# Kernel tuning notes

Measured on AMD Instinct MI355X. Metric: run time of the kernel, lower is better.

## Reference

```python
import jax, jax.numpy as jnp
import numpy as np

# ---- hardware / module constants (match init_kwargs) ----
IN_BITS = 8
OUT_PREC_BITS = 8
OUT_RANGE_BITS = 4
VMAX = 0.6                      # hardware_input_vmax
I_SCALE = 8020.0                # hardware_output_current_scaling
DAC_SCALE = 1.0 / 2 ** (IN_BITS - 1)
DAC_MAX = 2 ** (IN_BITS - 1)
DAC_MIN = -DAC_MAX
ADC_SCALE = 1.0 / 2 ** OUT_PREC_BITS
ADC_MAX = 2 ** (OUT_PREC_BITS + OUT_RANGE_BITS - 1)
ADC_MIN = -ADC_MAX
BW = 1e-08
KBT = 1.380649e-23 * 300.0
E_CONST = float(np.exp(1))
V_EPS = 1e-12                   # noise_minimum_voltage
WP = 3                          # weight_precision -> L = WP-1 bit levels
L = WP - 1
MI, MO = 128, 128               # memristor tile size
TJ, TK = 2, 2                   # input/output tiling (256/128)
OUT_FEATURES = 256


def fake_quant(x, scale, qmin, qmax):
    # torch.fake_quantize_per_tensor_affine with zero_point=0 (STE grads)
    q = jnp.round(x / scale)
    y = jnp.clip(q, qmin, qmax) * scale
    mask = (q >= qmin) & (q <= qmax)
    xg = jnp.where(mask, x, jax.lax.stop_gradient(x))
    return xg + jax.lax.stop_gradient(y - xg)


def poly_eval(c, x):
    # c: [2, P] ascending-degree coeffs (pos/neg stacked), x: [B,T,I] -> [2,B,T,I]
    # Horner form: same math as sum_p c_p * x**p, grad-safe at x == 0.
    acc = jnp.broadcast_to(c[:, -1][:, None, None, None], (2,) + x.shape)
    for p in range(c.shape[-1] - 2, -1, -1):
        acc = acc * x[None] + c[:, p][:, None, None, None]
    return acc


def _paired_array(cl, ch, r, v, noise):
    # cl:[2,Pl] ch:[2,Ph] r:[2,MI,MO] v:[B,T,MI] noise:[2,T,MI,MO]
    low = poly_eval(cl, v)[..., None]       # [2,B,T,MI,1]
    high = poly_eval(ch, v)[..., None]
    r_b = r[:, None, None]                  # [2,1,1,MI,MO]
    raw = low * (1.0 - r_b) + high * r_b    # [2,B,T,MI,MO]
    johnson = 4.0 * KBT * BW * jnp.abs(raw / (jnp.abs(v)[None, ..., None] + V_EPS))
    shot = 2.0 * E_CONST * jnp.abs(raw) * BW
    sigma = jnp.sqrt(johnson + shot)
    noised = raw + noise[:, None] * sigma   # noise broadcast over batch dim B
    out = jnp.sum(noised, axis=-2)          # reduce over I -> [2,B,T,MO]
    return out[0] - out[1]                  # paired (pos - neg) bitlines


def _forward(x, poly_low, poly_high, r, bias):
    v = fake_quant(x, DAC_SCALE, DAC_MIN, DAC_MAX) * VMAX   # DAC
    B, T, _ = x.shape
    out = jnp.zeros((B, T, TK * MO), x.dtype)
    for i, bit in enumerate(reversed(range(WP - 1))):
        for j in range(TJ):
            vj = v[..., j * MI:(j + 1) * MI]
            for k in range(TK):
                nkey = jax.random.fold_in(jax.random.key(42), i * TJ * TK + j * TK + k)
                noise = jax.random.normal(nkey, (2, T, MI, MO), x.dtype)
                pair = _paired_array(poly_low[i, j, k], poly_high[i, j, k], r[i, j, k], vj, noise)
                adc_out = fake_quant(pair * I_SCALE, ADC_SCALE, ADC_MIN, ADC_MAX)  # ADC
                out = out.at[..., k * MO:(k + 1) * MO].add(adc_out * (2.0 ** bit))
    return out[..., :OUT_FEATURES] + bias


def setup_inputs() -> dict:
    key = jax.random.key(0)
    ks = jax.random.split(key, 5)
    x = jax.random.normal(ks[0], (4, 256, 256), jnp.float32)
    poly_low = jax.random.normal(ks[1], (L, TJ, TK, 2, 7), jnp.float32) * 1e-3
    poly_high = jax.random.normal(ks[2], (L, TJ, TK, 2, 6), jnp.float32) * 1e-3
    r = jax.random.uniform(ks[3], (L, TJ, TK, 2, MI, MO), dtype=jnp.float32)
    bias = jax.random.normal(ks[4], (OUT_FEATURES,), jnp.float32) * 0.01
    return {"x": x, "poly_low": poly_low, "poly_high": poly_high, "r": r, "bias": bias}


def reference(x, poly_low, poly_high, r, bias):
    return _forward(x, poly_low, poly_high, r, bias)
```

## Files before the change

kernel.cpp:

```cpp
#include <hip/hip_runtime.h>
#include <stdint.h>


struct KeyPack { uint32_t k0[8]; uint32_t k1[8]; uint32_t k2[8]; };

#define TFR(r)  { x0 += x1; \
  x1 = __builtin_amdgcn_alignbit(x1, x1, 32u - (r)); x1 ^= x0; }
#define TFR3(r, kinj) { x0 = x0 + x1 + (kinj); \
  x1 = __builtin_amdgcn_alignbit(x1, x1, 32u - (r)); x1 ^= x0; }

__device__ __forceinline__ uint32_t tf_bits(uint32_t ks0, uint32_t ks1,
                                            uint32_t ks2, uint32_t x1) {
  uint32_t x0 = ks0;
  TFR(13) TFR(15) TFR(26) TFR(6)
  x1 += ks2 + 1u;
  TFR3(17, ks1) TFR(29) TFR(16) TFR(24)
  x1 += ks0 + 2u;
  TFR3(13, ks2) TFR(15) TFR(26) TFR(6)
  x1 += ks1 + 3u;
  TFR3(17, ks0) TFR(29) TFR(16) TFR(24)
  x1 += ks2 + 4u;
  TFR3(13, ks1) TFR(15) TFR(26) TFR(6)
  x0 += ks2; x1 += ks0 + 5u;
  return x0 ^ x1;
}

__host__ inline void threefry2x32_host(uint32_t k0, uint32_t k1,
                                       uint32_t x0, uint32_t x1,
                                       uint32_t& y0, uint32_t& y1) {
  const uint32_t ks0 = k0, ks1 = k1, ks2 = k0 ^ k1 ^ 0x1BD11BDAu;
  x0 += ks0; x1 += ks1;
#define TF_ROUND(r) { x0 += x1; x1 = (x1 << (r)) | (x1 >> (32 - (r))); x1 ^= x0; }
  TF_ROUND(13) TF_ROUND(15) TF_ROUND(26) TF_ROUND(6)
  x0 += ks1; x1 += ks2 + 1u;
  TF_ROUND(17) TF_ROUND(29) TF_ROUND(16) TF_ROUND(24)
  x0 += ks2; x1 += ks0 + 2u;
  TF_ROUND(13) TF_ROUND(15) TF_ROUND(26) TF_ROUND(6)
  x0 += ks0; x1 += ks1 + 3u;
  TF_ROUND(17) TF_ROUND(29) TF_ROUND(16) TF_ROUND(24)
  x0 += ks1; x1 += ks2 + 4u;
  TF_ROUND(13) TF_ROUND(15) TF_ROUND(26) TF_ROUND(6)
  x0 += ks2; x1 += ks0 + 5u;
#undef TF_ROUND
  y0 = x0; y1 = x1;
}

__device__ __forceinline__ float bits_to_nscaled(uint32_t bits) {
  float g = __uint_as_float(__builtin_amdgcn_alignbit(0x7Fu, bits, 9u));
  float u = fmaxf(fmaf(g, 2.0f, -3.0f), -0.99999994f);
  float l = __logf(fmaf(u, -u, 1.0f));
  float p;
  if (l > -5.0f) {
    float z = -2.5f - l;
    p =            -4.134083e-7f;
    p = fmaf(p, z, -1.377554e-6f);
    p = fmaf(p, z,  8.132747e-5f);
    p = fmaf(p, z,  4.950817e-4f);
  } else {
    float z = __builtin_amdgcn_sqrtf(-l) - 3.0f;
    p =            -2.513466e-6f;
    p = fmaf(p, z,  3.112373e-6f);
    p = fmaf(p, z,  3.302966e-4f);
    p = fmaf(p, z,  9.341406e-4f);
  }
  return p * u;
}

__global__ void memristor_init(const float* __restrict__ bias,
                               float* __restrict__ out) {
  int idx = blockIdx.x * 256 + threadIdx.x;
  out[idx] = bias[idx & 255];
}

__global__ __launch_bounds__(256, 4)
void memristor_main(const float* __restrict__ x,
                    const float* __restrict__ poly_low,
                    const float* __restrict__ poly_high,
                    const float* __restrict__ r,
                    float* __restrict__ out,
                    KeyPack keys) {
  __shared__ __align__(16) float LH[128][16];
  __shared__ float RED[128][9];

  const int tid = threadIdx.x;
  const int bid = blockIdx.x;
  const int c = bid >> 8;
  const int t = bid & 255;
  const int j = (c >> 1) & 1;
  const int k = c & 1;

  for (int task = tid; task < 1024; task += 256) {
    int pb = task & 7;
    int mi = task >> 3;
    int p = pb >> 2, b = pb & 3;
    float xv = x[(b * 256 + t) * 256 + j * 128 + mi];
    float q = rintf(xv * 128.0f);
    q = fminf(fmaxf(q, -128.0f), 128.0f);
    float v = (q * 0.0078125f) * 0.6f;
    const float* cl = poly_low + (c * 2 + p) * 7;
    float lo = cl[6];
    #pragma unroll
    for (int n = 5; n >= 0; --n) lo = fmaf(lo, v, cl[n]);
    const float* ch = poly_high + (c * 2 + p) * 6;
    float hi = ch[5];
    #pragma unroll
    for (int n = 4; n >= 0; --n) hi = fmaf(hi, v, ch[n]);
    LH[mi][pb] = lo;
    LH[mi][8 + pb] = hi - lo;
  }
  __syncthreads();

  const int mo = tid & 127;
  const int mih = tid >> 7;
  const int miBase = mih * 64;
  const uint32_t k0 = keys.k0[c], k1 = keys.k1[c], k2 = keys.k2[c];
  const float* r0p = r + c * 32768 + miBase * 128 + mo;
  const float* r1p = r0p + 16384;
  uint32_t sk = (uint32_t)(t * 16384 + miBase * 128 + mo) + k1;

  float acc[8];
  #pragma unroll
  for (int v2 = 0; v2 < 8; ++v2) acc[v2] = 0.0f;

  #pragma unroll 2
  for (int ii = 0; ii < 64; ++ii) {
    const float4* lh4 = (const float4*)(&LH[miBase + ii][0]);
    float4 L0 = lh4[0];
    float4 L1 = lh4[1];
    float4 D0 = lh4[2];
    float4 D1 = lh4[3];
    float r0 = r0p[ii * 128];
    float r1 = r1p[ii * 128];

    uint32_t b0 = tf_bits(k0, k1, k2, sk);
    uint32_t b1 = tf_bits(k0, k1, k2, sk + 4194304u);
    sk += 128u;
    float n0 = bits_to_nscaled(b0);
    float n1 = bits_to_nscaled(b1);

    float raw0 = fmaf(D0.x, r0, L0.x);
    float raw1 = fmaf(D0.y, r0, L0.y);
    float raw2 = fmaf(D0.z, r0, L0.z);
    float raw3 = fmaf(D0.w, r0, L0.w);
    float raw4 = fmaf(D1.x, r1, L1.x);
    float raw5 = fmaf(D1.y, r1, L1.y);
    float raw6 = fmaf(D1.z, r1, L1.z);
    float raw7 = fmaf(D1.w, r1, L1.w);

    float q0 = __builtin_amdgcn_sqrtf(fabsf(raw0));
    float q1 = __builtin_amdgcn_sqrtf(fabsf(raw1));
    float q2 = __builtin_amdgcn_sqrtf(fabsf(raw2));
    float q3 = __builtin_amdgcn_sqrtf(fabsf(raw3));
    float q4 = __builtin_amdgcn_sqrtf(fabsf(raw4));
    float q5 = __builtin_amdgcn_sqrtf(fabsf(raw5));
    float q6 = __builtin_amdgcn_sqrtf(fabsf(raw6));
    float q7 = __builtin_amdgcn_sqrtf(fabsf(raw7));

    acc[0] += fmaf(n0, q0, raw0);
    acc[1] += fmaf(n0, q1, raw1);
    acc[2] += fmaf(n0, q2, raw2);
    acc[3] += fmaf(n0, q3, raw3);
    acc[4] += fmaf(n1, q4, raw4);
    acc[5] += fmaf(n1, q5, raw5);
    acc[6] += fmaf(n1, q6, raw6);
    acc[7] += fmaf(n1, q7, raw7);
  }

  if (mih == 1) {
    #pragma unroll
    for (int v2 = 0; v2 < 8; ++v2) RED[mo][v2] = acc[v2];
  }
  __syncthreads();
  if (mih == 0) {
    #pragma unroll
    for (int v2 = 0; v2 < 8; ++v2) acc[v2] += RED[mo][v2];
    const float QSC = 2053120.0f;
    const float OSC = (c & 4) ? 0.00390625f : 0.0078125f;
    #pragma unroll
    for (int b = 0; b < 4; ++b) {
      float pair = acc[b] - acc[4 + b];
      float q = rintf(pair * QSC);
      q = fminf(fmaxf(q, -2048.0f), 2048.0f);
      atomicAdd(&out[(b * 256 + t) * 256 + k * 128 + mo], q * OSC);
    }
  }
}

extern "C" void kernel_launch(void* const* d_in, const int* in_sizes, int n_in,
                              void* d_out, int out_size, void* d_ws, size_t ws_size,
                              hipStream_t stream) {
  const float* x    = (const float*)d_in[0];
  const float* pl   = (const float*)d_in[1];
  const float* ph   = (const float*)d_in[2];
  const float* r    = (const float*)d_in[3];
  const float* bias = (const float*)d_in[4];
  float* out = (float*)d_out;

  KeyPack keys;
  for (uint32_t cc = 0; cc < 8; ++cc) {
    uint32_t y0, y1;
    threefry2x32_host(0u, 42u, 0u, cc, y0, y1);
    keys.k0[cc] = y0; keys.k1[cc] = y1;
    keys.k2[cc] = y0 ^ y1 ^ 0x1BD11BDAu;
  }

  memristor_init<<<1024, 256, 0, stream>>>(bias, out);
  memristor_main<<<2048, 256, 0, stream>>>(x, pl, ph, r, out, keys);
}
```

Before: 220.3 us.

## Pack four time steps per 1024-thread block and use log2-based inverse-erf

Each block now handles four consecutive time steps with 1024 threads instead of one with 256, so the grid shrinks from 2048 to 512 blocks and shared LH/RED buffers are replicated per sub-block. The same r tile is read by the four sub-blocks, which may improve cache reuse and lower launch overhead. Separately, the Gaussian noise transform now uses log2 directly with refit polynomial coefficients, dropping the offset subtraction in the central branch. Launch bounds of 1024 threads with min 4 blocks per unit may force tighter register limits, and the refit coefficients risk small numerical deviations.

```diff
diff --git a/kernel.cpp b/kernel.cpp
--- a/kernel.cpp
+++ b/kernel.cpp
@@ -48,20 +48,19 @@
 __device__ __forceinline__ float bits_to_nscaled(uint32_t bits) {
   float g = __uint_as_float(__builtin_amdgcn_alignbit(0x7Fu, bits, 9u));
   float u = fmaxf(fmaf(g, 2.0f, -3.0f), -0.99999994f);
-  float l = __logf(fmaf(u, -u, 1.0f));
+  float lam = __log2f(fmaf(u, -u, 1.0f));
   float p;
-  if (l > -5.0f) {
-    float z = -2.5f - l;
-    p =            -4.134083e-7f;
-    p = fmaf(p, z, -1.377554e-6f);
-    p = fmaf(p, z,  8.132747e-5f);
-    p = fmaf(p, z,  4.950817e-4f);
+  if (lam > -7.2134752f) {
+    p =              1.376760e-7f;
+    p = fmaf(p, lam, 8.278247e-7f);
+    p = fmaf(p, lam, -5.5773259e-5f);
+    p = fmaf(p, lam, 2.8961282e-4f);
   } else {
-    float z = __builtin_amdgcn_sqrtf(-l) - 3.0f;
-    p =            -2.513466e-6f;
-    p = fmaf(p, z,  3.112373e-6f);
-    p = fmaf(p, z,  3.302966e-4f);
-    p = fmaf(p, z,  9.341406e-4f);
+    float m = __builtin_amdgcn_sqrtf(-lam);
+    p =            -1.450466e-6f;
+    p = fmaf(p, m,  1.783712e-5f);
+    p = fmaf(p, m,  2.0294250e-4f);
+    p = fmaf(p, m,  3.9125739e-5f);
   }
   return p * u;
 }
@@ -72,28 +71,29 @@
   out[idx] = bias[idx & 255];
 }
 
-__global__ __launch_bounds__(256, 4)
+__global__ __launch_bounds__(1024, 4)
 void memristor_main(const float* __restrict__ x,
                     const float* __restrict__ poly_low,
                     const float* __restrict__ poly_high,
                     const float* __restrict__ r,
                     float* __restrict__ out,
                     KeyPack keys) {
-  __shared__ __align__(16) float LH[128][16];
-  __shared__ float RED[128][9];
+  __shared__ __align__(16) float LH[4][128][16];
+  __shared__ float RED[4][128][9];
 
   const int tid = threadIdx.x;
   const int bid = blockIdx.x;
-  const int c = bid >> 8;
-  const int t = bid & 255;
+  const int c = bid >> 6;
+  const int tBase = (bid & 63) * 4;
   const int j = (c >> 1) & 1;
   const int k = c & 1;
 
-  for (int task = tid; task < 1024; task += 256) {
+  for (int task = tid; task < 4096; task += 1024) {
     int pb = task & 7;
-    int mi = task >> 3;
+    int mi = (task >> 3) & 127;
+    int sb = task >> 10;
     int p = pb >> 2, b = pb & 3;
-    float xv = x[(b * 256 + t) * 256 + j * 128 + mi];
+    float xv = x[(b * 256 + tBase + sb) * 256 + j * 128 + mi];
     float q = rintf(xv * 128.0f);
     q = fminf(fmaxf(q, -128.0f), 128.0f);
     float v = (q * 0.0078125f) * 0.6f;
@@ -105,13 +105,16 @@
     float hi = ch[5];
     #pragma unroll
     for (int n = 4; n >= 0; --n) hi = fmaf(hi, v, ch[n]);
-    LH[mi][pb] = lo;
-    LH[mi][8 + pb] = hi - lo;
+    LH[sb][mi][pb] = lo;
+    LH[sb][mi][8 + pb] = hi - lo;
   }
   __syncthreads();
 
-  const int mo = tid & 127;
-  const int mih = tid >> 7;
+  const int sb  = tid >> 8;
+  const int tl  = tid & 255;
+  const int t   = tBase + sb;
+  const int mo  = tl & 127;
+  const int mih = tl >> 7;
   const int miBase = mih * 64;
   const uint32_t k0 = keys.k0[c], k1 = keys.k1[c], k2 = keys.k2[c];
   const float* r0p = r + c * 32768 + miBase * 128 + mo;
@@ -124,7 +127,7 @@
 
   #pragma unroll 2
   for (int ii = 0; ii < 64; ++ii) {
-    const float4* lh4 = (const float4*)(&LH[miBase + ii][0]);
+    const float4* lh4 = (const float4*)(&LH[sb][miBase + ii][0]);
     float4 L0 = lh4[0];
     float4 L1 = lh4[1];
     float4 D0 = lh4[2];
@@ -168,12 +171,12 @@
 
   if (mih == 1) {
     #pragma unroll
-    for (int v2 = 0; v2 < 8; ++v2) RED[mo][v2] = acc[v2];
+    for (int v2 = 0; v2 < 8; ++v2) RED[sb][mo][v2] = acc[v2];
   }
   __syncthreads();
   if (mih == 0) {
     #pragma unroll
-    for (int v2 = 0; v2 < 8; ++v2) acc[v2] += RED[mo][v2];
+    for (int v2 = 0; v2 < 8; ++v2) acc[v2] += RED[sb][mo][v2];
     const float QSC = 2053120.0f;
     const float OSC = (c & 4) ? 0.00390625f : 0.0078125f;
     #pragma unroll
@@ -205,5 +208,5 @@
   }
 
   memristor_init<<<1024, 256, 0, stream>>>(bias, out);
-  memristor_main<<<2048, 256, 0, stream>>>(x, pl, ph, r, out, keys);
-}
+  memristor_main<<<512, 1024, 0, stream>>>(x, pl, ph, r, out, keys);
+}
```

Result: no change. 217.7 us (-1.1%).
